# Optimization experiments

Measured on AMD Instinct MI355X. Metric: run time of the kernel, lower is better.

The kernel has to match this reference:

```python
import jax, jax.numpy as jnp
import numpy as np

B = 16384  # batch
D = 1024   # input_size (== hidden_size, required by the original code)
H = 1024   # hidden_size


def setup_inputs() -> dict:
    key = jax.random.key(0)
    ks = jax.random.split(key, 20)
    s = 0.02
    inp = {
        "x": jax.random.normal(ks[0], (B, D), dtype=jnp.float32),
        "h": jax.random.normal(ks[1], (B, H), dtype=jnp.float32),
        "c_prev": jax.random.normal(ks[2], (B, H), dtype=jnp.float32),
    }
    names = ["i_x", "f_x", "c_x", "o_x", "i_h", "f_h", "c_h", "o_h"]
    for n, name in enumerate(names):
        in_dim = D if name.endswith("_x") else H
        inp["W" + name] = jax.random.normal(ks[3 + 2 * n], (H, in_dim), dtype=jnp.float32) * s
        inp["b" + name] = jax.random.normal(ks[4 + 2 * n], (H,), dtype=jnp.float32) * s
    return inp


def reference(x, h, c_prev,
              Wi_x, bi_x, Wf_x, bf_x, Wc_x, bc_x, Wo_x, bo_x,
              Wi_h, bi_h, Wf_h, bf_h, Wc_h, bc_h, Wo_h, bo_h):
    # NOTE: the original module applies NO sigmoid to the gates; i, f, o are raw affine sums.
    i = x @ Wi_x.T + bi_x + h @ Wi_h.T + bi_h
    f = x @ Wf_x.T + bf_x + h @ Wf_h.T + bf_h
    g = jnp.tanh(x @ Wc_x.T + bc_x + h @ Wc_h.T + bc_h)
    o = x @ Wo_x.T + bo_x + h @ Wo_h.T + bo_h
    c_next = g * i + c_prev * f
    h_next = o * jnp.tanh(c_next)
    return (h_next, c_next)
```

## Files before the change

kernel.cpp:

```cpp
#include <hip/hip_runtime.h>
#include <hip/hip_bf16.h>


#define MROWS 16384
#define NCOLS 1024
#define KTOT  2048

typedef __attribute__((ext_vector_type(8))) short bf16x8;
typedef __attribute__((ext_vector_type(4))) float f32x4;
typedef unsigned int u32;
typedef unsigned short u16;

__device__ __forceinline__ u16 f2bf(float f) {
  union { float f; u32 u; } v; v.f = f;
  u32 r = v.u + 0x7fffu + ((v.u >> 16) & 1u);
  return (u16)(r >> 16);
}

__device__ __forceinline__ bf16x8 pack8(float4 lo, float4 hi) {
  bf16x8 v;
  v[0] = (short)f2bf(lo.x); v[1] = (short)f2bf(lo.y);
  v[2] = (short)f2bf(lo.z); v[3] = (short)f2bf(lo.w);
  v[4] = (short)f2bf(hi.x); v[5] = (short)f2bf(hi.y);
  v[6] = (short)f2bf(hi.z); v[7] = (short)f2bf(hi.w);
  return v;
}

__device__ __forceinline__ float tanh_fast(float x) {
  float e = __expf(2.0f * x);
  return 1.0f - 2.0f / (e + 1.0f);
}

typedef __attribute__((address_space(1))) const u32 gas_u32;
typedef __attribute__((address_space(3))) u32 las_u32;

__device__ __forceinline__ void gl_lds16(const void* g, void* l) {
  __builtin_amdgcn_global_load_lds((gas_u32*)g, (las_u32*)l, 16, 0, 0);
}

__global__ void __launch_bounds__(256) convAW(
    const float* __restrict__ x, const float* __restrict__ h,
    const float* __restrict__ wix, const float* __restrict__ wfx,
    const float* __restrict__ wcx, const float* __restrict__ wox,
    const float* __restrict__ wih, const float* __restrict__ wfh,
    const float* __restrict__ wch, const float* __restrict__ woh,
    u16* __restrict__ A, u16* __restrict__ W) {
  if (blockIdx.x < 4096u) {
    u32 t = blockIdx.x * 256u + threadIdx.x;
    #pragma unroll
    for (int i = 0; i < 4; ++i) {
      u32 chunk = t + (u32)i * 1048576u;
      u32 row = chunk >> 8;
      u32 cpos = (chunk & 255u) * 8u;
      const float* src = (cpos < 1024u) ? (x + (size_t)row * 1024 + cpos)
                                        : (h + (size_t)row * 1024 + (cpos - 1024u));
      float4 lo = *(const float4*)src;
      float4 hi = *(const float4*)(src + 4);
      *(bf16x8*)(A + (size_t)chunk * 8) = pack8(lo, hi);
    }
  } else {
    u32 t = (blockIdx.x - 4096u) * 256u + threadIdx.x;
    const float* WX[4] = {wix, wfx, wcx, wox};
    const float* WH[4] = {wih, wfh, wch, woh};
    #pragma unroll
    for (int g = 0; g < 4; ++g) {
      u32 n = t >> 8;
      u32 cpos = (t & 255u) * 8u;
      const float* src = (cpos < 1024u) ? (WX[g] + (size_t)n * 1024 + cpos)
                                        : (WH[g] + (size_t)n * 1024 + (cpos - 1024u));
      float4 lo = *(const float4*)src;
      float4 hi = *(const float4*)(src + 4);
      *(bf16x8*)(W + (size_t)g * 2097152 + (size_t)t * 8) = pack8(lo, hi);
    }
  }
}

__global__ void __launch_bounds__(256) lstm_g128(
    const u16* __restrict__ Abf, const u16* __restrict__ Wbf,
    const float* __restrict__ bix, const float* __restrict__ bfx,
    const float* __restrict__ bcx, const float* __restrict__ box_,
    const float* __restrict__ bih, const float* __restrict__ bfh,
    const float* __restrict__ bch, const float* __restrict__ boh,
    const float* __restrict__ cprev, float* __restrict__ out) {
  __shared__ alignas(16) u16 sA[8192];
  __shared__ alignas(16) u16 sB[8192];

  const u32 tid = threadIdx.x;
  const u32 lane = tid & 63u;
  const u32 wid = tid >> 6;
  const u32 wr = wid >> 1, wc = wid & 1u;
  const u32 l15 = lane & 15u, l4 = lane >> 4;
  const u32 r = lane >> 3, k8 = lane & 7u;
  const u32 col16 = k8 ^ r;

  const u32 bidx = blockIdx.x;
  const u32 sid = (bidx & 7u) * 512u + (bidx >> 3);
  const u32 bm = sid >> 5, bn = sid & 31u;

  const u16* gAp[4];
  const u16* gBp[4];
  #pragma unroll
  for (int j = 0; j < 4; ++j) {
    gAp[j] = Abf + (size_t)(bm * 128u + wid * 32u + (u32)j * 8u + r) * KTOT + col16 * 8u;
    u32 q = wid * 4u + (u32)j;
    u32 Wrow = ((q >> 1) & 3u) * 1024u + bn * 32u + (wid >> 1) * 16u + 8u * (q & 1u) + r;
    gBp[j] = Wbf + (size_t)Wrow * KTOT + col16 * 8u;
  }

#define STAGE(ktile) do { \
    _Pragma("unroll") \
    for (int j = 0; j < 4; ++j) { \
      gl_lds16(gAp[j] + (u32)(ktile) * 64u, sA + (wid * 4u + (u32)j) * 512u); \
      gl_lds16(gBp[j] + (u32)(ktile) * 64u, sB + (wid * 4u + (u32)j) * 512u); \
    } \
  } while (0)

  const char* cA = (const char*)sA;
  const char* cB = (const char*)sB;

  f32x4 acc[4][4];
  #pragma unroll
  for (int g = 0; g < 4; ++g)
    #pragma unroll
    for (int m = 0; m < 4; ++m)
      acc[g][m] = (f32x4){0.f, 0.f, 0.f, 0.f};

  for (int kt = 0; kt < KTOT / 64; ++kt) {
    if (kt) __syncthreads();
    STAGE(kt);
    __syncthreads();

    #pragma unroll
    for (int s = 0; s < 2; ++s) {
      bf16x8 af[4];
      #pragma unroll
      for (int m = 0; m < 4; ++m) {
        u32 mrow = wr * 64u + (u32)m * 16u + l15;
        u32 off = mrow * 128u + (((u32)s * 64u + l4 * 16u) ^ ((mrow & 7u) << 4));
        af[m] = *(const bf16x8*)(cA + off);
      }
      #pragma unroll
      for (int g = 0; g < 4; ++g) {
        u32 frow = wc * 64u + (u32)g * 16u + l15;
        u32 off = frow * 128u + (((u32)s * 64u + l4 * 16u) ^ ((frow & 7u) << 4));
        bf16x8 bfr = *(const bf16x8*)(cB + off);
        #pragma unroll
        for (int m = 0; m < 4; ++m)
          acc[g][m] = __builtin_amdgcn_mfma_f32_16x16x32_bf16(af[m], bfr, acc[g][m], 0, 0, 0);
      }
    }
  }
#undef STAGE

  const u32 col = bn * 32u + wc * 16u + l15;
  const float bi = bix[col] + bih[col];
  const float bff = bfx[col] + bfh[col];
  const float bc = bcx[col] + bch[col];
  const float bo = box_[col] + boh[col];
  #pragma unroll
  for (int m = 0; m < 4; ++m) {
    u32 row0 = bm * 128u + wr * 64u + (u32)m * 16u + l4 * 4u;
    #pragma unroll
    for (int rr = 0; rr < 4; ++rr) {
      size_t idx = (size_t)(row0 + (u32)rr) * 1024 + col;
      float iv = acc[0][m][rr] + bi;
      float fv = acc[1][m][rr] + bff;
      float gv = tanh_fast(acc[2][m][rr] + bc);
      float ov = acc[3][m][rr] + bo;
      float cp = cprev[idx];
      float cn = gv * iv + cp * fv;
      out[idx] = ov * tanh_fast(cn);
      out[(size_t)16777216 + idx] = cn;
    }
  }
}

__global__ void __launch_bounds__(256, 2) lstm_gemm_fb(
    const float* __restrict__ x, const float* __restrict__ h,
    const float* __restrict__ wix, const float* __restrict__ wfx,
    const float* __restrict__ wcx, const float* __restrict__ wox,
    const float* __restrict__ wih, const float* __restrict__ wfh,
    const float* __restrict__ wch, const float* __restrict__ woh,
    const float* __restrict__ bix, const float* __restrict__ bfx,
    const float* __restrict__ bcx, const float* __restrict__ box_,
    const float* __restrict__ bih, const float* __restrict__ bfh,
    const float* __restrict__ bch, const float* __restrict__ boh,
    const float* __restrict__ cprev, float* __restrict__ out) {
  __shared__ alignas(16) u16 sA[128 * 64];
  __shared__ alignas(16) u16 sB[4 * 64 * 64];
  const u32 tid = threadIdx.x;
  const u32 lane = tid & 63u;
  const u32 wid = tid >> 6;
  const u32 wr = wid >> 1, wc = wid & 1u;
  const u32 bidx = blockIdx.x;
  const u32 bm = bidx >> 4, bn = bidx & 15u;
  f32x4 acc[4][4][2];
  #pragma unroll
  for (int g = 0; g < 4; ++g)
    #pragma unroll
    for (int m = 0; m < 4; ++m)
      #pragma unroll
      for (int n = 0; n < 2; ++n)
        acc[g][m][n] = (f32x4){0.f, 0.f, 0.f, 0.f};
  const u32 l15 = lane & 15u, l4 = lane >> 4;
  for (int kt = 0; kt < KTOT / 64; ++kt) {
    const u32 k0 = (u32)kt * 64u;
    if (kt) __syncthreads();
    #pragma unroll
    for (int c = 0; c < 4; ++c) {
      u32 chunk = tid + (u32)c * 256u;
      u32 row = chunk >> 3;
      u32 cp = (chunk & 7u) * 8u;
      u32 gk = k0 + cp;
      const float* src = (gk < 1024u) ? (x + (size_t)(bm * 128u + row) * 1024 + gk)
                                      : (h + (size_t)(bm * 128u + row) * 1024 + (gk - 1024u));
      float4 lo = *(const float4*)src;
      float4 hi = *(const float4*)(src + 4);
      u32 dst = row * 128u + ((cp * 2u) ^ ((row & 7u) << 4));
      *(bf16x8*)((char*)sA + dst) = pack8(lo, hi);
    }
    #pragma unroll
    for (int g = 0; g < 4; ++g) {
      const float* Wxg = (g == 0) ? wix : (g == 1) ? wfx : (g == 2) ? wcx : wox;
      const float* Whg = (g == 0) ? wih : (g == 1) ? wfh : (g == 2) ? wch : woh;
      #pragma unroll
      for (int cc = 0; cc < 2; ++cc) {
        u32 c3 = tid + (u32)cc * 256u;
        u32 row = c3 >> 3;
        u32 cp = (c3 & 7u) * 8u;
        u32 gk = k0 + cp;
        const float* src = (gk < 1024u) ? (Wxg + (size_t)(bn * 64u + row) * 1024 + gk)
                                        : (Whg + (size_t)(bn * 64u + row) * 1024 + (gk - 1024u));
        float4 lo = *(const float4*)src;
        float4 hi = *(const float4*)(src + 4);
        u32 dst = (u32)g * 8192u + row * 128u + ((cp * 2u) ^ ((row & 7u) << 4));
        *(bf16x8*)((char*)sB + dst) = pack8(lo, hi);
      }
    }
    __syncthreads();
    #pragma unroll
    for (int s = 0; s < 2; ++s) {
      bf16x8 af[4];
      #pragma unroll
      for (int m = 0; m < 4; ++m) {
        u32 mrow = wr * 64u + (u32)m * 16u + l15;
        u32 off = mrow * 128u + (((u32)s * 64u + l4 * 16u) ^ ((mrow & 7u) << 4));
        af[m] = *(const bf16x8*)((const char*)sA + off);
      }
      #pragma unroll
      for (int g = 0; g < 4; ++g) {
        #pragma unroll
        for (int nf = 0; nf < 2; ++nf) {
          u32 nrow = wc * 32u + (u32)nf * 16u + l15;
          u32 off = (u32)g * 8192u + nrow * 128u +
                    (((u32)s * 64u + l4 * 16u) ^ ((nrow & 7u) << 4));
          bf16x8 bfr = *(const bf16x8*)((const char*)sB + off);
          #pragma unroll
          for (int m = 0; m < 4; ++m)
            acc[g][m][nf] = __builtin_amdgcn_mfma_f32_16x16x32_bf16(af[m], bfr, acc[g][m][nf], 0, 0, 0);
        }
      }
    }
  }
  #pragma unroll
  for (int nf = 0; nf < 2; ++nf) {
    u32 col = bn * 64u + wc * 32u + (u32)nf * 16u + l15;
    float bi = bix[col] + bih[col];
    float bff = bfx[col] + bfh[col];
    float bc = bcx[col] + bch[col];
    float bo = box_[col] + boh[col];
    #pragma unroll
    for (int m = 0; m < 4; ++m) {
      u32 row0 = bm * 128u + wr * 64u + (u32)m * 16u + l4 * 4u;
      #pragma unroll
      for (int rr = 0; rr < 4; ++rr) {
        size_t idx = (size_t)(row0 + (u32)rr) * 1024 + col;
        float iv = acc[0][m][nf][rr] + bi;
        float fv = acc[1][m][nf][rr] + bff;
        float gv = tanh_fast(acc[2][m][nf][rr] + bc);
        float ov = acc[3][m][nf][rr] + bo;
        float cp = cprev[idx];
        float cn = gv * iv + cp * fv;
        out[idx] = ov * tanh_fast(cn);
        out[(size_t)16777216 + idx] = cn;
      }
    }
  }
}

extern "C" void kernel_launch(void* const* d_in, const int* in_sizes, int n_in,
                              void* d_out, int out_size, void* d_ws, size_t ws_size,
                              hipStream_t stream) {
  const float* x = (const float*)d_in[0];
  const float* h = (const float*)d_in[1];
  const float* cprev = (const float*)d_in[2];
  const float* wix = (const float*)d_in[3];  const float* bix = (const float*)d_in[4];
  const float* wfx = (const float*)d_in[5];  const float* bfx = (const float*)d_in[6];
  const float* wcx = (const float*)d_in[7];  const float* bcx = (const float*)d_in[8];
  const float* wox = (const float*)d_in[9];  const float* box_ = (const float*)d_in[10];
  const float* wih = (const float*)d_in[11]; const float* bih = (const float*)d_in[12];
  const float* wfh = (const float*)d_in[13]; const float* bfh = (const float*)d_in[14];
  const float* wch = (const float*)d_in[15]; const float* bch = (const float*)d_in[16];
  const float* woh = (const float*)d_in[17]; const float* boh = (const float*)d_in[18];
  float* out = (float*)d_out;

  const size_t needA = (size_t)MROWS * KTOT * 2;
  const size_t needW = (size_t)4 * NCOLS * KTOT * 2;

  if (ws_size >= needA + needW) {
    u16* Abf = (u16*)d_ws;
    u16* Wbf = (u16*)((char*)d_ws + needA);
    convAW<<<dim3(5120), dim3(256), 0, stream>>>(
        x, h, wix, wfx, wcx, wox, wih, wfh, wch, woh, Abf, Wbf);
    lstm_g128<<<dim3(4096), dim3(256), 0, stream>>>(
        Abf, Wbf, bix, bfx, bcx, box_, bih, bfh, bch, boh, cprev, out);
  } else {
    lstm_gemm_fb<<<dim3(2048), dim3(256), 0, stream>>>(
        x, h, wix, wfx, wcx, wox, wih, wfh, wch, woh,
        bix, bfx, bcx, box_, bih, bfh, bch, boh, cprev, out);
  }
}
```

Measured before the change: 375.7 us.

## Switch LSTM GEMM to 32x32x16 MFMA with 128x256 block tile

Replaces the 16x16x32 MFMA kernel with one using 32x32x16 bf16 MFMA and a larger block tile: 128 rows by 64 output columns across all four gates, for 256 weight rows per block. The grid halves to 2048 blocks and the block-index swizzle is dropped. The aim is more operand reuse per LDS load and fewer LDS reads per FLOP. It also adds s_setprio around the MFMA section and launch_bounds(256,2). The larger LDS footprint, higher register use and loss of the L2-friendly swizzle could reduce occupancy or cache locality.

```diff
diff --git a/kernel.cpp b/kernel.cpp
--- a/kernel.cpp
+++ b/kernel.cpp
@@ -7,7 +7,7 @@
 #define KTOT  2048
 
 typedef __attribute__((ext_vector_type(8))) short bf16x8;
-typedef __attribute__((ext_vector_type(4))) float f32x4;
+typedef __attribute__((ext_vector_type(16))) float f32x16;
 typedef unsigned int u32;
 typedef unsigned short u16;
 
@@ -75,98 +75,107 @@
   }
 }
 
-__global__ void __launch_bounds__(256) lstm_g128(
+__global__ void __launch_bounds__(256, 2) lstm_g32(
     const u16* __restrict__ Abf, const u16* __restrict__ Wbf,
     const float* __restrict__ bix, const float* __restrict__ bfx,
     const float* __restrict__ bcx, const float* __restrict__ box_,
     const float* __restrict__ bih, const float* __restrict__ bfh,
     const float* __restrict__ bch, const float* __restrict__ boh,
     const float* __restrict__ cprev, float* __restrict__ out) {
-  __shared__ alignas(16) u16 sA[8192];
-  __shared__ alignas(16) u16 sB[8192];
+  __shared__ alignas(16) u16 sA[128 * 64];
+  __shared__ alignas(16) u16 sB[256 * 64];
 
   const u32 tid = threadIdx.x;
   const u32 lane = tid & 63u;
   const u32 wid = tid >> 6;
   const u32 wr = wid >> 1, wc = wid & 1u;
-  const u32 l15 = lane & 15u, l4 = lane >> 4;
-  const u32 r = lane >> 3, k8 = lane & 7u;
-  const u32 col16 = k8 ^ r;
+  const u32 l31 = lane & 31u, l5 = lane >> 5;
 
   const u32 bidx = blockIdx.x;
-  const u32 sid = (bidx & 7u) * 512u + (bidx >> 3);
-  const u32 bm = sid >> 5, bn = sid & 31u;
+  const u32 bm = bidx >> 4, bn = bidx & 15u;
 
   const u16* gAp[4];
-  const u16* gBp[4];
+  const u16* gBp[8];
   #pragma unroll
   for (int j = 0; j < 4; ++j) {
-    gAp[j] = Abf + (size_t)(bm * 128u + wid * 32u + (u32)j * 8u + r) * KTOT + col16 * 8u;
-    u32 q = wid * 4u + (u32)j;
-    u32 Wrow = ((q >> 1) & 3u) * 1024u + bn * 32u + (wid >> 1) * 16u + 8u * (q & 1u) + r;
-    gBp[j] = Wbf + (size_t)Wrow * KTOT + col16 * 8u;
+    u32 c = (wid * 4u + (u32)j) * 64u + lane;
+    u32 row = c >> 3, k8 = c & 7u;
+    gAp[j] = Abf + (size_t)(bm * 128u + row) * KTOT + (k8 ^ (row & 7u)) * 8u;
+  }
+  #pragma unroll
+  for (int j = 0; j < 8; ++j) {
+    u32 c = (wid * 8u + (u32)j) * 64u + lane;
+    u32 fr = c >> 3, k8 = c & 7u;
+    u32 Wrow = ((fr >> 5) & 3u) * 1024u + bn * 64u + (fr >> 7) * 32u + (fr & 31u);
+    gBp[j] = Wbf + (size_t)Wrow * KTOT + (k8 ^ (fr & 7u)) * 8u;
   }
 
 #define STAGE(ktile) do { \
     _Pragma("unroll") \
-    for (int j = 0; j < 4; ++j) { \
+    for (int j = 0; j < 4; ++j) \
       gl_lds16(gAp[j] + (u32)(ktile) * 64u, sA + (wid * 4u + (u32)j) * 512u); \
-      gl_lds16(gBp[j] + (u32)(ktile) * 64u, sB + (wid * 4u + (u32)j) * 512u); \
-    } \
+    _Pragma("unroll") \
+    for (int j = 0; j < 8; ++j) \
+      gl_lds16(gBp[j] + (u32)(ktile) * 64u, sB + (wid * 8u + (u32)j) * 512u); \
   } while (0)
 
   const char* cA = (const char*)sA;
   const char* cB = (const char*)sB;
 
-  f32x4 acc[4][4];
+  f32x16 acc[4][2];
   #pragma unroll
   for (int g = 0; g < 4; ++g)
     #pragma unroll
-    for (int m = 0; m < 4; ++m)
-      acc[g][m] = (f32x4){0.f, 0.f, 0.f, 0.f};
+    for (int mt = 0; mt < 2; ++mt)
+      acc[g][mt] = (f32x16)(0.f);
+
+  const u32 mrow0 = wr * 64u + l31;
+  const u32 brow0 = wc * 128u + l31;
 
   for (int kt = 0; kt < KTOT / 64; ++kt) {
-    if (kt) __syncthreads();
     STAGE(kt);
     __syncthreads();
 
-    #pragma unroll
-    for (int s = 0; s < 2; ++s) {
-      bf16x8 af[4];
-      #pragma unroll
-      for (int m = 0; m < 4; ++m) {
-        u32 mrow = wr * 64u + (u32)m * 16u + l15;
-        u32 off = mrow * 128u + (((u32)s * 64u + l4 * 16u) ^ ((mrow & 7u) << 4));
-        af[m] = *(const bf16x8*)(cA + off);
+    __builtin_amdgcn_s_setprio(1);
+    #pragma unroll
+    for (int ks = 0; ks < 4; ++ks) {
+      const u32 kc = (u32)ks * 2u + l5;
+      bf16x8 a0, a1;
+      {
+        u32 r0 = mrow0;
+        a0 = *(const bf16x8*)(cA + r0 * 128u + ((kc ^ (r0 & 7u)) << 4));
+        u32 r1 = mrow0 + 32u;
+        a1 = *(const bf16x8*)(cA + r1 * 128u + ((kc ^ (r1 & 7u)) << 4));
       }
       #pragma unroll
       for (int g = 0; g < 4; ++g) {
-        u32 frow = wc * 64u + (u32)g * 16u + l15;
-        u32 off = frow * 128u + (((u32)s * 64u + l4 * 16u) ^ ((frow & 7u) << 4));
-        bf16x8 bfr = *(const bf16x8*)(cB + off);
-        #pragma unroll
-        for (int m = 0; m < 4; ++m)
-          acc[g][m] = __builtin_amdgcn_mfma_f32_16x16x32_bf16(af[m], bfr, acc[g][m], 0, 0, 0);
-      }
-    }
+        u32 br = brow0 + (u32)g * 32u;
+        bf16x8 bfr = *(const bf16x8*)(cB + br * 128u + ((kc ^ (br & 7u)) << 4));
+        acc[g][0] = __builtin_amdgcn_mfma_f32_32x32x16_bf16(a0, bfr, acc[g][0], 0, 0, 0);
+        acc[g][1] = __builtin_amdgcn_mfma_f32_32x32x16_bf16(a1, bfr, acc[g][1], 0, 0, 0);
+      }
+    }
+    __builtin_amdgcn_s_setprio(0);
+    __syncthreads();
   }
 #undef STAGE
 
-  const u32 col = bn * 32u + wc * 16u + l15;
+  const u32 col = bn * 64u + wc * 32u + l31;
   const float bi = bix[col] + bih[col];
   const float bff = bfx[col] + bfh[col];
   const float bc = bcx[col] + bch[col];
   const float bo = box_[col] + boh[col];
   #pragma unroll
-  for (int m = 0; m < 4; ++m) {
-    u32 row0 = bm * 128u + wr * 64u + (u32)m * 16u + l4 * 4u;
-    #pragma unroll
-    for (int rr = 0; rr < 4; ++rr) {
-      size_t idx = (size_t)(row0 + (u32)rr) * 1024 + col;
-      float iv = acc[0][m][rr] + bi;
-      float fv = acc[1][m][rr] + bff;
-      float gv = tanh_fast(acc[2][m][rr] + bc);
-      float ov = acc[3][m][rr] + bo;
+  for (int mt = 0; mt < 2; ++mt) {
+    const u32 rbase = bm * 128u + wr * 64u + (u32)mt * 32u + 4u * l5;
+    #pragma unroll
+    for (int reg = 0; reg < 16; ++reg) {
+      u32 row = rbase + (u32)(reg & 3) + 8u * (u32)(reg >> 2);
+      size_t idx = (size_t)row * 1024 + col;
+      float iv = acc[0][mt][reg] + bi;
+      float fv = acc[1][mt][reg] + bff;
+      float gv = tanh_fast(acc[2][mt][reg] + bc);
+      float ov = acc[3][mt][reg] + bo;
       float cp = cprev[idx];
       float cn = gv * iv + cp * fv;
       out[idx] = ov * tanh_fast(cn);
@@ -186,6 +195,7 @@
     const float* __restrict__ bih, const float* __restrict__ bfh,
     const float* __restrict__ bch, const float* __restrict__ boh,
     const float* __restrict__ cprev, float* __restrict__ out) {
+  typedef __attribute__((ext_vector_type(4))) float f32x4;
   __shared__ alignas(16) u16 sA[128 * 64];
   __shared__ alignas(16) u16 sB[4 * 64 * 64];
   const u32 tid = threadIdx.x;
@@ -312,7 +322,7 @@
     u16* Wbf = (u16*)((char*)d_ws + needA);
     convAW<<<dim3(5120), dim3(256), 0, stream>>>(
         x, h, wix, wfx, wcx, wox, wih, wfh, wch, woh, Abf, Wbf);
-    lstm_g128<<<dim3(4096), dim3(256), 0, stream>>>(
+    lstm_g32<<<dim3(2048), dim3(256), 0, stream>>>(
         Abf, Wbf, bix, bfx, bcx, box_, bih, bfh, bch, boh, cprev, out);
   } else {
     lstm_gemm_fb<<<dim3(2048), dim3(256), 0, stream>>>(
```

After: 348.2 us. 7.3% less time.
